# Kernel optimization log

Measured on AMD Instinct MI355X. Metric: run time of the kernel, lower is better.

The kernel has to match this reference:

```python
import jax, jax.numpy as jnp
import numpy as np

B, C, H = 128, 3, 224
PATCH_NUM, PS = 14, 16          # patch_size = image_size / patch_num
NP = PATCH_NUM * PATCH_NUM      # 196 patches
TOP_K = 20
D = 768                         # ViT-B hidden dim
NUM_CLASSES = 1000


def setup_inputs() -> dict:
    key = jax.random.key(0)
    k1, k2, k3, k4, k5 = jax.random.split(key, 5)
    return {
        "inputs": jax.random.normal(k1, (B, C, H, H), jnp.float32),
        "patch_grad": jax.random.normal(k2, (B, NP, D), jnp.float32),
        "attack_w": jax.random.uniform(k3, (C, H, H), jnp.float32),  # torch.rand init
        "w_cls": jax.random.normal(k4, (C * NP, NUM_CLASSES), jnp.float32) * 0.02,
        "targets": jax.random.randint(k5, (B,), 0, NUM_CLASSES),
    }


def reference(inputs, patch_grad, attack_w, w_cls, targets):
    # --- top-k patch selection from patch-embedding gradients ---
    # sum over batch, then over embedding dim -> [NP]
    sum_patch = patch_grad.sum(axis=0).sum(axis=1)
    _, top_idx = jax.lax.top_k(sum_patch, TOP_K)  # distinct patch indices

    # --- vectorized equivalent of the per-pixel double loop ---
    # patch (ix, iy) -> pixel block [ix*PS:(ix+1)*PS, iy*PS:(iy+1)*PS]
    ix = top_idx // PATCH_NUM
    iy = top_idx % PATCH_NUM
    mask_p = jnp.zeros((PATCH_NUM, PATCH_NUM), inputs.dtype).at[ix, iy].set(1.0)
    mask = jnp.kron(mask_p, jnp.ones((PS, PS), inputs.dtype))  # [H, H] pixel mask
    x = inputs + mask[None, None, :, :] * attack_w[None, :, :, :]  # [B,C,H,H]

    # --- surrogate classifier head (stand-in for aux_vit second forward) ---
    # per-patch average pool, flatten, linear -> logits [B, NUM_CLASSES]
    pooled = x.reshape(B, C, PATCH_NUM, PS, PATCH_NUM, PS).mean(axis=(3, 5))
    logits = pooled.reshape(B, -1) @ w_cls

    targets_prob = jax.nn.softmax(logits, axis=1)
    # original applies CrossEntropyLoss to the *probabilities* (treats them as logits)
    logp = jax.nn.log_softmax(targets_prob, axis=1)
    ce = -jnp.take_along_axis(logp, targets[:, None], axis=1)[:, 0]  # [B]

    u = 0.0
    l2loss = jnp.mean(attack_w * attack_w)
    loss = u * l2loss - (1.0 - u) * ce.mean()
    return targets_prob, loss
```

## Files before the change

### kernel.cpp

```cpp
#include <hip/hip_runtime.h>
#include <math.h>

#define PA_OFF    0
#define APOOL_OFF 25600
#define MA_OFF    26624
#define IPOOL_OFF 28672
#define PL_OFF    106496

__device__ __forceinline__ float hsum(float4 v) { return (v.x + v.y) + (v.z + v.w); }

__global__ __launch_bounds__(256, 4) void k1_main(
    const float* __restrict__ inputs,
    const float* __restrict__ patch_grad,
    const float* __restrict__ attack_w,
    float* __restrict__ ws)
{
  const int bid  = blockIdx.x;
  const int lane = threadIdx.x & 63;

  if (bid < 784) {
    const int w  = bid * 4 + (threadIdx.x >> 6);
    const int R0 = w * 8;
    const float4* src = (const float4*)patch_grad + (size_t)R0 * 192 + lane;

    float4 va[6], vb[6];
    #pragma unroll
    for (int j = 0; j < 6; ++j) va[j] = src[(size_t)j * 64];
    __builtin_amdgcn_sched_barrier(0);
    #pragma unroll
    for (int j = 0; j < 6; ++j) vb[j] = src[(size_t)(6 + j) * 64];
    __builtin_amdgcn_sched_barrier(0);

    float s[8];
    s[0] = hsum(va[0]) + hsum(va[1]) + hsum(va[2]);
    s[1] = hsum(va[3]) + hsum(va[4]) + hsum(va[5]);
    #pragma unroll
    for (int j = 0; j < 6; ++j) va[j] = src[(size_t)(12 + j) * 64];
    __builtin_amdgcn_sched_barrier(0);
    s[2] = hsum(vb[0]) + hsum(vb[1]) + hsum(vb[2]);
    s[3] = hsum(vb[3]) + hsum(vb[4]) + hsum(vb[5]);
    #pragma unroll
    for (int j = 0; j < 6; ++j) vb[j] = src[(size_t)(18 + j) * 64];
    __builtin_amdgcn_sched_barrier(0);
    s[4] = hsum(va[0]) + hsum(va[1]) + hsum(va[2]);
    s[5] = hsum(va[3]) + hsum(va[4]) + hsum(va[5]);
    s[6] = hsum(vb[0]) + hsum(vb[1]) + hsum(vb[2]);
    s[7] = hsum(vb[3]) + hsum(vb[4]) + hsum(vb[5]);

    #pragma unroll
    for (int o = 32; o > 0; o >>= 1) {
      #pragma unroll
      for (int k = 0; k < 8; ++k) s[k] += __shfl_down(s[k], o, 64);
    }
    if (lane == 0) {
      float* pa = ws + PA_OFF;
      #pragma unroll
      for (int k = 0; k < 8; ++k) {
        const int row = R0 + k, b = row / 196, p = row - b * 196;
        pa[p * 128 + b] = s[k];
      }
    }
  } else {
    const int w = (bid - 784) * 4 + (threadIdx.x >> 6);
    if (w >= 5418) return;
    const int img = w / 14, px = w - img * 14;
    const float* base = (img < 384)
        ? inputs + (size_t)img * 50176
        : attack_w + (size_t)(img - 384) * 50176;
    const float* src = base + px * 3584;
    const int cl = (lane < 56) ? lane : 55;

    float4 v[8], u[8];
    #pragma unroll
    for (int r = 0; r < 8; ++r) v[r] = *(const float4*)(src + r * 224 + cl * 4);
    __builtin_amdgcn_sched_barrier(0);
    #pragma unroll
    for (int r = 0; r < 8; ++r) u[r] = *(const float4*)(src + (8 + r) * 224 + cl * 4);
    __builtin_amdgcn_sched_barrier(0);

    float4 s = make_float4(0.f, 0.f, 0.f, 0.f);
    #pragma unroll
    for (int r = 0; r < 8; ++r) {
      s.x += v[r].x + u[r].x; s.y += v[r].y + u[r].y;
      s.z += v[r].z + u[r].z; s.w += v[r].w + u[r].w;
    }
    s.x += __shfl_xor(s.x, 1); s.y += __shfl_xor(s.y, 1);
    s.z += __shfl_xor(s.z, 1); s.w += __shfl_xor(s.w, 1);
    s.x += __shfl_xor(s.x, 2); s.y += __shfl_xor(s.y, 2);
    s.z += __shfl_xor(s.z, 2); s.w += __shfl_xor(s.w, 2);
    if ((lane & 3) == 0 && lane < 56) {
      const int py = lane >> 2;
      const float ps = ((s.x + s.y) + (s.z + s.w)) * (1.f / 256.f);
      if (img < 384) {
        const int b = img / 3, c = img - b * 3;
        ws[IPOOL_OFF + (size_t)b * 588 + c * 196 + px * 14 + py] = ps;
      } else {
        ws[APOOL_OFF + (img - 384) * 196 + px * 14 + py] = ps;
      }
    }
  }
}

__global__ __launch_bounds__(256) void k2_topk(float* __restrict__ ws,
                                               float* __restrict__ d_loss)
{
  __shared__ float sp[196];
  __shared__ float maskp[196];
  const int t = threadIdx.x;
  if (t < 196) {
    const float4* q = (const float4*)(ws + PA_OFF + (size_t)t * 128);
    float4 a = make_float4(0.f, 0.f, 0.f, 0.f);
    #pragma unroll
    for (int j = 0; j < 32; ++j) {
      const float4 v = q[j];
      a.x += v.x; a.y += v.y; a.z += v.z; a.w += v.w;
    }
    sp[t] = (a.x + a.y) + (a.z + a.w);
  }
  if (t == 0) *d_loss = 0.f;
  __syncthreads();
  if (t < 196) {
    const float v = sp[t];
    int cnt = 0;
    for (int j = 0; j < 196; ++j) {
      const float u = sp[j];
      cnt += (u > v || (u == v && j < t)) ? 1 : 0;
    }
    maskp[t] = (cnt < 20) ? 1.f : 0.f;
  }
  __syncthreads();
  for (int k = t; k < 588; k += 256) {
    const int p = k % 196;
    ws[MA_OFF + k] = maskp[p] * ws[APOOL_OFF + k];
  }
}

__global__ __launch_bounds__(256) void k3_gemm(const float* __restrict__ w_cls,
                                               float* __restrict__ ws)
{
  __shared__ __align__(16) float lp[147 * 8];
  const int bid = blockIdx.x;
  const int ks = bid & 3;
  const int nt = (bid >> 2) & 15;
  const int bg = bid >> 6;
  const int t  = threadIdx.x;
  const float* ipool = ws + IPOOL_OFF;
  const float* ma    = ws + MA_OFF;
  for (int idx = t; idx < 1176; idx += 256) {
    const int bb = idx / 147;
    const int kk = idx - bb * 147;
    const int k  = ks * 147 + kk;
    lp[kk * 8 + bb] = ipool[(size_t)(bg * 8 + bb) * 588 + k] + ma[k];
  }
  __syncthreads();
  const int lane = t & 63, g = t >> 6;
  const int n = nt * 64 + lane;
  const bool valid = n < 1000;
  float a0 = 0, a1 = 0;
  const float* wc = w_cls + (size_t)ks * 147 * 1000 + n;
  #pragma unroll 21
  for (int kk = 0; kk < 147; ++kk) {
    const float w = valid ? wc[(size_t)kk * 1000] : 0.f;
    const float2 pv = *(const float2*)&lp[kk * 8 + g * 2];
    a0 += pv.x * w; a1 += pv.y * w;
  }
  float* pl = ws + PL_OFF;
  const int rowb = ks * 128 + bg * 8 + g * 2;
  pl[(size_t)(rowb + 0) * 1024 + n] = a0;
  pl[(size_t)(rowb + 1) * 1024 + n] = a1;
}

__global__ __launch_bounds__(256) void k4_softmax(const float* __restrict__ ws,
                                                  const int* __restrict__ targets,
                                                  float* __restrict__ out)
{
  __shared__ float red[4];
  __shared__ float sh_pt;
  const int b = blockIdx.x, t = threadIdx.x;
  const float* pl = ws + PL_OFF;
  float l[4]; bool val[4];
  #pragma unroll
  for (int j = 0; j < 4; ++j) {
    const int n = j * 256 + t;
    val[j] = (n < 1000);
    float s = -INFINITY;
    if (val[j]) {
      s = 0.f;
      #pragma unroll
      for (int ks = 0; ks < 4; ++ks) s += pl[(size_t)(ks * 128 + b) * 1024 + n];
    }
    l[j] = s;
  }
  float m = fmaxf(fmaxf(l[0], l[1]), fmaxf(l[2], l[3]));
  #pragma unroll
  for (int o = 32; o > 0; o >>= 1) m = fmaxf(m, __shfl_down(m, o, 64));
  if ((t & 63) == 0) red[t >> 6] = m;
  __syncthreads();
  const float m1 = fmaxf(fmaxf(red[0], red[1]), fmaxf(red[2], red[3]));
  __syncthreads();
  float e[4]; float s = 0.f;
  #pragma unroll
  for (int j = 0; j < 4; ++j) { e[j] = val[j] ? expf(l[j] - m1) : 0.f; s += e[j]; }
  #pragma unroll
  for (int o = 32; o > 0; o >>= 1) s += __shfl_down(s, o, 64);
  if ((t & 63) == 0) red[t >> 6] = s;
  __syncthreads();
  const float S1 = red[0] + red[1] + red[2] + red[3];
  __syncthreads();
  const float inv = 1.f / S1;
  const int tgt = targets[b];
  float p[4];
  #pragma unroll
  for (int j = 0; j < 4; ++j) {
    const int n = j * 256 + t;
    if (val[j]) {
      p[j] = e[j] * inv;
      out[(size_t)b * 1000 + n] = p[j];
      if (n == tgt) sh_pt = p[j];
    } else {
      p[j] = -INFINITY;
    }
  }
  float m2 = fmaxf(fmaxf(p[0], p[1]), fmaxf(p[2], p[3]));
  #pragma unroll
  for (int o = 32; o > 0; o >>= 1) m2 = fmaxf(m2, __shfl_down(m2, o, 64));
  if ((t & 63) == 0) red[t >> 6] = m2;
  __syncthreads();
  const float M2 = fmaxf(fmaxf(red[0], red[1]), fmaxf(red[2], red[3]));
  __syncthreads();
  float s2 = 0.f;
  #pragma unroll
  for (int j = 0; j < 4; ++j) s2 += val[j] ? expf(p[j] - M2) : 0.f;
  #pragma unroll
  for (int o = 32; o > 0; o >>= 1) s2 += __shfl_down(s2, o, 64);
  if ((t & 63) == 0) red[t >> 6] = s2;
  __syncthreads();
  if (t == 0) {
    const float S2 = red[0] + red[1] + red[2] + red[3];
    const float lse2 = M2 + logf(S2);
    atomicAdd(out + 128000, (sh_pt - lse2) * (1.f / 128.f));
  }
}

extern "C" void kernel_launch(void* const* d_in, const int* in_sizes, int n_in,
                              void* d_out, int out_size, void* d_ws, size_t ws_size,
                              hipStream_t stream) {
  const float* inputs     = (const float*)d_in[0];
  const float* patch_grad = (const float*)d_in[1];
  const float* attack_w   = (const float*)d_in[2];
  const float* w_cls      = (const float*)d_in[3];
  const int*   targets    = (const int*)d_in[4];
  float* out = (float*)d_out;
  float* ws  = (float*)d_ws;

  hipLaunchKernelGGL(k1_main,  dim3(2139), dim3(256), 0, stream,
                     inputs, patch_grad, attack_w, ws);
  hipLaunchKernelGGL(k2_topk,  dim3(1),    dim3(256), 0, stream, ws, out + 128000);
  hipLaunchKernelGGL(k3_gemm,  dim3(1024), dim3(256), 0, stream, w_cls, ws);
  hipLaunchKernelGGL(k4_softmax, dim3(128), dim3(256), 0, stream, ws, targets, out);
}
```

Measured before the change: 205.3 us.

## Issue all streaming loads at once with nontemporal hints; drop GEMM split-K

The reduction kernel now issues all 24 (or 16) vector loads per wave up front as nontemporal loads instead of double-buffered batches, and lowers the occupancy hint to 2 to make room for the extra registers. The classifier GEMM no longer splits K into four partial products, so each block covers the full 588-long reduction and the softmax kernel reads one logit row directly. This removes the partial-sum writes and reads, but it leaves fewer GEMM blocks (256) with longer serial loops, and the lower occupancy may reduce latency hiding in the bandwidth-bound first kernel.

```diff
diff --git a/kernel.cpp b/kernel.cpp
--- a/kernel.cpp
+++ b/kernel.cpp
@@ -7,9 +7,11 @@
 #define IPOOL_OFF 28672
 #define PL_OFF    106496
 
-__device__ __forceinline__ float hsum(float4 v) { return (v.x + v.y) + (v.z + v.w); }
-
-__global__ __launch_bounds__(256, 4) void k1_main(
+typedef float v4f __attribute__((ext_vector_type(4)));
+
+__device__ __forceinline__ float hsum4(v4f v) { return (v.x + v.y) + (v.z + v.w); }
+
+__global__ __launch_bounds__(256, 2) void k1_main(
     const float* __restrict__ inputs,
     const float* __restrict__ patch_grad,
     const float* __restrict__ attack_w,
@@ -21,31 +23,18 @@
   if (bid < 784) {
     const int w  = bid * 4 + (threadIdx.x >> 6);
     const int R0 = w * 8;
-    const float4* src = (const float4*)patch_grad + (size_t)R0 * 192 + lane;
-
-    float4 va[6], vb[6];
-    #pragma unroll
-    for (int j = 0; j < 6; ++j) va[j] = src[(size_t)j * 64];
+    const v4f* src = (const v4f*)patch_grad + (size_t)R0 * 192 + lane;
+
+    v4f v[24];
+    #pragma unroll
+    for (int j = 0; j < 24; ++j)
+      v[j] = __builtin_nontemporal_load(src + (size_t)j * 64);
     __builtin_amdgcn_sched_barrier(0);
-    #pragma unroll
-    for (int j = 0; j < 6; ++j) vb[j] = src[(size_t)(6 + j) * 64];
-    __builtin_amdgcn_sched_barrier(0);
 
     float s[8];
-    s[0] = hsum(va[0]) + hsum(va[1]) + hsum(va[2]);
-    s[1] = hsum(va[3]) + hsum(va[4]) + hsum(va[5]);
-    #pragma unroll
-    for (int j = 0; j < 6; ++j) va[j] = src[(size_t)(12 + j) * 64];
-    __builtin_amdgcn_sched_barrier(0);
-    s[2] = hsum(vb[0]) + hsum(vb[1]) + hsum(vb[2]);
-    s[3] = hsum(vb[3]) + hsum(vb[4]) + hsum(vb[5]);
-    #pragma unroll
-    for (int j = 0; j < 6; ++j) vb[j] = src[(size_t)(18 + j) * 64];
-    __builtin_amdgcn_sched_barrier(0);
-    s[4] = hsum(va[0]) + hsum(va[1]) + hsum(va[2]);
-    s[5] = hsum(va[3]) + hsum(va[4]) + hsum(va[5]);
-    s[6] = hsum(vb[0]) + hsum(vb[1]) + hsum(vb[2]);
-    s[7] = hsum(vb[3]) + hsum(vb[4]) + hsum(vb[5]);
+    #pragma unroll
+    for (int k = 0; k < 8; ++k)
+      s[k] = hsum4(v[3 * k]) + hsum4(v[3 * k + 1]) + hsum4(v[3 * k + 2]);
 
     #pragma unroll
     for (int o = 32; o > 0; o >>= 1) {
@@ -67,23 +56,18 @@
     const float* base = (img < 384)
         ? inputs + (size_t)img * 50176
         : attack_w + (size_t)(img - 384) * 50176;
-    const float* src = base + px * 3584;
+    const v4f* src = (const v4f*)(base + px * 3584);
     const int cl = (lane < 56) ? lane : 55;
 
-    float4 v[8], u[8];
-    #pragma unroll
-    for (int r = 0; r < 8; ++r) v[r] = *(const float4*)(src + r * 224 + cl * 4);
+    v4f v[16];
+    #pragma unroll
+    for (int r = 0; r < 16; ++r)
+      v[r] = __builtin_nontemporal_load(src + r * 56 + cl);
     __builtin_amdgcn_sched_barrier(0);
-    #pragma unroll
-    for (int r = 0; r < 8; ++r) u[r] = *(const float4*)(src + (8 + r) * 224 + cl * 4);
-    __builtin_amdgcn_sched_barrier(0);
-
-    float4 s = make_float4(0.f, 0.f, 0.f, 0.f);
-    #pragma unroll
-    for (int r = 0; r < 8; ++r) {
-      s.x += v[r].x + u[r].x; s.y += v[r].y + u[r].y;
-      s.z += v[r].z + u[r].z; s.w += v[r].w + u[r].w;
-    }
+
+    v4f s = v[0];
+    #pragma unroll
+    for (int r = 1; r < 16; ++r) s += v[r];
     s.x += __shfl_xor(s.x, 1); s.y += __shfl_xor(s.y, 1);
     s.z += __shfl_xor(s.z, 1); s.w += __shfl_xor(s.w, 1);
     s.x += __shfl_xor(s.x, 2); s.y += __shfl_xor(s.y, 2);
@@ -138,34 +122,32 @@
 __global__ __launch_bounds__(256) void k3_gemm(const float* __restrict__ w_cls,
                                                float* __restrict__ ws)
 {
-  __shared__ __align__(16) float lp[147 * 8];
+  __shared__ __align__(16) float lp[588 * 8];
   const int bid = blockIdx.x;
-  const int ks = bid & 3;
-  const int nt = (bid >> 2) & 15;
-  const int bg = bid >> 6;
+  const int nt = bid & 15;
+  const int bg = bid >> 4;
   const int t  = threadIdx.x;
   const float* ipool = ws + IPOOL_OFF;
   const float* ma    = ws + MA_OFF;
-  for (int idx = t; idx < 1176; idx += 256) {
-    const int bb = idx / 147;
-    const int kk = idx - bb * 147;
-    const int k  = ks * 147 + kk;
-    lp[kk * 8 + bb] = ipool[(size_t)(bg * 8 + bb) * 588 + k] + ma[k];
+  for (int idx = t; idx < 4704; idx += 256) {
+    const int bb = idx / 588;
+    const int kk = idx - bb * 588;
+    lp[kk * 8 + bb] = ipool[(size_t)(bg * 8 + bb) * 588 + kk] + ma[kk];
   }
   __syncthreads();
   const int lane = t & 63, g = t >> 6;
   const int n = nt * 64 + lane;
   const bool valid = n < 1000;
   float a0 = 0, a1 = 0;
-  const float* wc = w_cls + (size_t)ks * 147 * 1000 + n;
-  #pragma unroll 21
-  for (int kk = 0; kk < 147; ++kk) {
+  const float* wc = w_cls + n;
+  #pragma unroll 7
+  for (int kk = 0; kk < 588; ++kk) {
     const float w = valid ? wc[(size_t)kk * 1000] : 0.f;
     const float2 pv = *(const float2*)&lp[kk * 8 + g * 2];
     a0 += pv.x * w; a1 += pv.y * w;
   }
   float* pl = ws + PL_OFF;
-  const int rowb = ks * 128 + bg * 8 + g * 2;
+  const int rowb = bg * 8 + g * 2;
   pl[(size_t)(rowb + 0) * 1024 + n] = a0;
   pl[(size_t)(rowb + 1) * 1024 + n] = a1;
 }
@@ -177,19 +159,13 @@
   __shared__ float red[4];
   __shared__ float sh_pt;
   const int b = blockIdx.x, t = threadIdx.x;
-  const float* pl = ws + PL_OFF;
+  const float* pl = ws + PL_OFF + (size_t)b * 1024;
   float l[4]; bool val[4];
   #pragma unroll
   for (int j = 0; j < 4; ++j) {
     const int n = j * 256 + t;
     val[j] = (n < 1000);
-    float s = -INFINITY;
-    if (val[j]) {
-      s = 0.f;
-      #pragma unroll
-      for (int ks = 0; ks < 4; ++ks) s += pl[(size_t)(ks * 128 + b) * 1024 + n];
-    }
-    l[j] = s;
+    l[j] = val[j] ? pl[n] : -INFINITY;
   }
   float m = fmaxf(fmaxf(l[0], l[1]), fmaxf(l[2], l[3]));
   #pragma unroll
@@ -256,6 +232,6 @@
   hipLaunchKernelGGL(k1_main,  dim3(2139), dim3(256), 0, stream,
                      inputs, patch_grad, attack_w, ws);
   hipLaunchKernelGGL(k2_topk,  dim3(1),    dim3(256), 0, stream, ws, out + 128000);
-  hipLaunchKernelGGL(k3_gemm,  dim3(1024), dim3(256), 0, stream, w_cls, ws);
+  hipLaunchKernelGGL(k3_gemm,  dim3(256),  dim3(256), 0, stream, w_cls, ws);
   hipLaunchKernelGGL(k4_softmax, dim3(128), dim3(256), 0, stream, ws, targets, out);
 }
```

After: 235.7 us. +14.8%, slower.
